# Kernel optimization log

Hardware: AMD Instinct MI355X
Metric: run time of the kernel (lower is better)

## Reference

```python
import jax, jax.numpy as jnp
import numpy as np
import math

NEG = -1000000.0

def setup_inputs() -> dict:
    key = jax.random.key(0)
    k1, k2, k3, k4 = jax.random.split(key, 4)
    B, S, D = 64, 1024, 64
    query = jax.random.normal(k1, (B, S, D), dtype=jnp.float32)
    key_t = jax.random.normal(k2, (B, S, D), dtype=jnp.float32)
    value = jax.random.normal(k3, (B, S, D), dtype=jnp.float32)
    valid_lens = jax.random.randint(k4, (B,), 1, S + 1, dtype=jnp.int32)
    return {"query": query, "key": key_t, "value": value, "valid_lens": valid_lens}

def reference(query, key, value, valid_lens):
    # query/key/value: [B, S, D]; valid_lens: [B]
    d = query.shape[-1]
    scores = jnp.einsum('bqd,bkd->bqk', query, key) / math.sqrt(d)
    Sk = key.shape[1]
    # 1D valid_lens -> same mask for every query row (repeat_interleave semantics)
    mask = jnp.arange(Sk)[None, None, :] < valid_lens[:, None, None]  # [B,1,Sk]
    scores = jnp.where(mask, scores, NEG)
    weights = jax.nn.softmax(scores, axis=-1)
    # dropout p=0.0 -> identity
    return jnp.einsum('bqk,bkd->bqd', weights, value)
```

## Files before the change

### kernel.cpp

```cpp
#include <hip/hip_runtime.h>
#include <hip/hip_bf16.h>
#include <cstdint>


typedef __attribute__((ext_vector_type(8))) short short8;
typedef __attribute__((ext_vector_type(4))) float f32x4;

#define B_   64
#define S_   1024
#define D_   64
#define BQ   64
#define BK   64
#define KPAD 72

__device__ __forceinline__ uint32_t pk2(float a, float b) {
    float2 t; t.x = a; t.y = b;
    union { __hip_bfloat162 h; uint32_t u; } c;
    c.h = __float22bfloat162_rn(t);
    return c.u;
}

__global__ __launch_bounds__(256, 4)
void attn_fwd(const float* __restrict__ Q, const float* __restrict__ K,
              const float* __restrict__ V, const int* __restrict__ VL,
              float* __restrict__ Out) {
    __shared__ __align__(16) unsigned short lK [BK * KPAD];
    __shared__ __align__(16) unsigned short lVt[D_ * 64];
    __shared__ __align__(16) unsigned short lP [4 * 16 * KPAD];
    __shared__ int sRank[64];

    const int tid  = threadIdx.x;
    const int wave = tid >> 6;
    const int lane = tid & 63;
    const int col  = lane & 15;
    const int quad = lane >> 4;

    const int g  = blockIdx.x;
    const int x  = g & 7;
    const int w  = g >> 3;
    const int pm = x * 4 + (w & 3);
    const int q0 = (w >> 2) * BQ;

    if (tid < 64) {
        const int myv = VL[tid];
        int r = 0;
        #pragma unroll 1
        for (int j = 0; j < 64; ++j) {
            const int vj = __shfl(myv, j, 64);
            r += (vj > myv) || (vj == myv && j < tid);
        }
        sRank[r] = tid;
    }
    __syncthreads();
    const int bA = sRank[pm];
    const int bB = sRank[63 - pm];

    const int T  = tid >> 4;
    const int m  = tid & 15;
    const int Tl = T & 3;
    const int cb = T >> 2;
    const int dcs = m >> 1;
    const int sws = ((dcs & 1) << 2) | (dcs >> 1);

    const float cexp = 0.18033688011112042f;
    unsigned short* pw = &lP[wave * 16 * KPAD];

    #pragma unroll 1
    for (int side = 0; side < 2; ++side) {
        const int b    = side ? bB : bA;
        const int vlen = VL[b];
        const int ntiles = (vlen + BK - 1) / BK;

        const float* Kb = K + (size_t)b * S_ * D_ + 4 * m;
        const float* Vb = V + (size_t)b * S_ * D_ + 4 * m;

        float4 kr[4], vr[4];
        #pragma unroll
        for (int j = 0; j < 4; ++j) {
            const int row = 2 * T + (j >> 1) * 32 + (j & 1);
            kr[j] = *(const float4*)(Kb + (size_t)row * D_);
            vr[j] = *(const float4*)(Vb + (size_t)row * D_);
        }

        short8 qa[2];
        {
            const int qrow = q0 + wave * 16 + col;
            const float* qp = Q + ((size_t)b * S_ + qrow) * D_ + quad * 8;
            #pragma unroll
            for (int c = 0; c < 2; ++c) {
                float4 x0 = *(const float4*)(qp + c * 32);
                float4 x1 = *(const float4*)(qp + c * 32 + 4);
                union { uint32_t u[4]; short8 s; } qq;
                qq.u[0] = pk2(x0.x, x0.y);
                qq.u[1] = pk2(x0.z, x0.w);
                qq.u[2] = pk2(x1.x, x1.y);
                qq.u[3] = pk2(x1.z, x1.w);
                qa[c] = qq.s;
            }
        }

        f32x4 ofrag[4];
        #pragma unroll
        for (int dt = 0; dt < 4; ++dt) ofrag[dt] = (f32x4){0.f, 0.f, 0.f, 0.f};
        float lsum = 0.f;

        #pragma unroll 1
        for (int kt = 0; kt < ntiles; ++kt) {
            const int kbase = kt * BK;

            __syncthreads();

            #pragma unroll
            for (int j = 0; j < 4; ++j) {
                const int row = 2 * T + (j >> 1) * 32 + (j & 1);
                uint2 kv;
                kv.x = pk2(kr[j].x, kr[j].y);
                kv.y = pk2(kr[j].z, kr[j].w);
                *(uint2*)&lK[row * KPAD + 4 * m] = kv;
            }
            #pragma unroll
            for (int i = 0; i < 2; ++i) {
                const int p = (cb + 4 * i) ^ sws;
                unsigned short* base = &lVt[p * 8 + 2 * Tl];
                const float4 va = vr[2 * i], vb2 = vr[2 * i + 1];
                *(uint32_t*)&base[(4 * m + 0) * 64] = pk2(va.x, vb2.x);
                *(uint32_t*)&base[(4 * m + 1) * 64] = pk2(va.y, vb2.y);
                *(uint32_t*)&base[(4 * m + 2) * 64] = pk2(va.z, vb2.z);
                *(uint32_t*)&base[(4 * m + 3) * 64] = pk2(va.w, vb2.w);
            }

            if (kt + 1 < ntiles) {
                const size_t off = (size_t)(kt + 1) * BK * D_;
                #pragma unroll
                for (int j = 0; j < 4; ++j) {
                    const int row = 2 * T + (j >> 1) * 32 + (j & 1);
                    kr[j] = *(const float4*)(Kb + off + (size_t)row * D_);
                    vr[j] = *(const float4*)(Vb + off + (size_t)row * D_);
                }
            }

            __syncthreads();

            f32x4 sfrag[4];
            #pragma unroll
            for (int ct = 0; ct < 4; ++ct) {
                f32x4 acc = (f32x4){0.f, 0.f, 0.f, 0.f};
                #pragma unroll
                for (int c = 0; c < 2; ++c) {
                    short8 kf = *(const short8*)&lK[(ct * 16 + col) * KPAD + c * 32 + quad * 8];
                    acc = __builtin_amdgcn_mfma_f32_16x16x32_bf16(kf, qa[c], acc, 0, 0, 0);
                }
                sfrag[ct] = acc;
            }

            if (kbase + BK <= vlen) {
                #pragma unroll
                for (int ct = 0; ct < 4; ++ct) {
                    float e0 = __builtin_amdgcn_exp2f(sfrag[ct][0] * cexp);
                    float e1 = __builtin_amdgcn_exp2f(sfrag[ct][1] * cexp);
                    float e2 = __builtin_amdgcn_exp2f(sfrag[ct][2] * cexp);
                    float e3 = __builtin_amdgcn_exp2f(sfrag[ct][3] * cexp);
                    lsum += (e0 + e1) + (e2 + e3);
                    uint2 pk; pk.x = pk2(e0, e1); pk.y = pk2(e2, e3);
                    *(uint2*)&pw[col * KPAD + ct * 16 + quad * 4] = pk;
                }
            } else {
                #pragma unroll
                for (int ct = 0; ct < 4; ++ct) {
                    const int kv0 = kbase + ct * 16 + quad * 4;
                    float e[4];
                    #pragma unroll
                    for (int rr = 0; rr < 4; ++rr) {
                        e[rr] = (kv0 + rr < vlen)
                              ? __builtin_amdgcn_exp2f(sfrag[ct][rr] * cexp) : 0.0f;
                        lsum += e[rr];
                    }
                    uint2 pk; pk.x = pk2(e[0], e[1]); pk.y = pk2(e[2], e[3]);
                    *(uint2*)&pw[col * KPAD + ct * 16 + quad * 4] = pk;
                }
            }

            #pragma unroll
            for (int kc = 0; kc < 2; ++kc) {
                short8 pa = *(const short8*)&pw[col * KPAD + kc * 32 + quad * 8];
                #pragma unroll
                for (int dt = 0; dt < 4; ++dt) {
                    const int sr = ((col >> 3) << 2) | dt;
                    const int p  = (kc * 4 + quad) ^ sr;
                    short8 vb = *(const short8*)&lVt[(dt * 16 + col) * 64 + p * 8];
                    ofrag[dt] = __builtin_amdgcn_mfma_f32_16x16x32_bf16(pa, vb, ofrag[dt], 0, 0, 0);
                }
            }
        }

        float s = lsum;
        s += __shfl_xor(s, 16, 64);
        s += __shfl_xor(s, 32, 64);
        const int qrow0 = q0 + wave * 16 + quad * 4;
        #pragma unroll
        for (int rr = 0; rr < 4; ++rr) {
            const float inv = 1.0f / __shfl(s, quad * 4 + rr, 64);
            float* op = Out + ((size_t)b * S_ + qrow0 + rr) * D_ + col;
            #pragma unroll
            for (int dt = 0; dt < 4; ++dt)
                op[dt * 16] = ofrag[dt][rr] * inv;
        }
    }
}

extern "C" void kernel_launch(void* const* d_in, const int* in_sizes, int n_in,
                              void* d_out, int out_size, void* d_ws, size_t ws_size,
                              hipStream_t stream) {
    const float* Q  = (const float*)d_in[0];
    const float* K  = (const float*)d_in[1];
    const float* V  = (const float*)d_in[2];
    const int*   VL = (const int*)d_in[3];
    float* Out = (float*)d_out;
    dim3 grid(B_ * (S_ / BQ) / 2);
    attn_fwd<<<grid, 256, 0, stream>>>(Q, K, V, VL, Out);
}
```

Baseline: 119.2 us.

## Split paired-batch blocks into one batch per block and double the grid

Each block used to process two batches (the longest and the shortest, chosen by valid_len rank) one after the other. Now each block handles a single batch, and the grid doubles to 1024 blocks. The new index mapping still interleaves batches by rank. The prefetch of the next K/V tile moves after the second barrier, and the tile loop is no longer marked unroll 1. Smaller blocks give the scheduler more freedom, but load balance now relies on hardware scheduling rather than explicit pairing.

```diff
diff --git a/kernel.cpp b/kernel.cpp
--- a/kernel.cpp
+++ b/kernel.cpp
@@ -35,12 +35,6 @@
     const int col  = lane & 15;
     const int quad = lane >> 4;
 
-    const int g  = blockIdx.x;
-    const int x  = g & 7;
-    const int w  = g >> 3;
-    const int pm = x * 4 + (w & 3);
-    const int q0 = (w >> 2) * BQ;
-
     if (tid < 64) {
         const int myv = VL[tid];
         int r = 0;
@@ -52,159 +46,159 @@
         sRank[r] = tid;
     }
     __syncthreads();
-    const int bA = sRank[pm];
-    const int bB = sRank[63 - pm];
+
+    const int g    = blockIdx.x;
+    const int x    = g & 7;
+    const int c    = (g >> 3) & 31;
+    const int s    = g >> 8;
+    const int m    = 4 * x + (c & 3);
+    const int b    = (s & 1) ? sRank[63 - m] : sRank[m];
+    const int q0   = ((c >> 2) + 8 * (s >> 1)) * BQ;
+    const int vlen = VL[b];
+    const int ntiles = (vlen + BK - 1) / BK;
 
     const int T  = tid >> 4;
-    const int m  = tid & 15;
+    const int md = tid & 15;
     const int Tl = T & 3;
     const int cb = T >> 2;
-    const int dcs = m >> 1;
+    const int dcs = md >> 1;
     const int sws = ((dcs & 1) << 2) | (dcs >> 1);
+
+    const float* Kb = K + (size_t)b * S_ * D_ + 4 * md;
+    const float* Vb = V + (size_t)b * S_ * D_ + 4 * md;
+
+    float4 kr[4], vr[4];
+    #pragma unroll
+    for (int j = 0; j < 4; ++j) {
+        const int row = 2 * T + (j >> 1) * 32 + (j & 1);
+        kr[j] = *(const float4*)(Kb + (size_t)row * D_);
+        vr[j] = *(const float4*)(Vb + (size_t)row * D_);
+    }
+
+    short8 qa[2];
+    {
+        const int qrow = q0 + wave * 16 + col;
+        const float* qp = Q + ((size_t)b * S_ + qrow) * D_ + quad * 8;
+        #pragma unroll
+        for (int cc = 0; cc < 2; ++cc) {
+            float4 x0 = *(const float4*)(qp + cc * 32);
+            float4 x1 = *(const float4*)(qp + cc * 32 + 4);
+            union { uint32_t u[4]; short8 s8; } qq;
+            qq.u[0] = pk2(x0.x, x0.y);
+            qq.u[1] = pk2(x0.z, x0.w);
+            qq.u[2] = pk2(x1.x, x1.y);
+            qq.u[3] = pk2(x1.z, x1.w);
+            qa[cc] = qq.s8;
+        }
+    }
+
+    f32x4 ofrag[4];
+    #pragma unroll
+    for (int dt = 0; dt < 4; ++dt) ofrag[dt] = (f32x4){0.f, 0.f, 0.f, 0.f};
+    float lsum = 0.f;
 
     const float cexp = 0.18033688011112042f;
     unsigned short* pw = &lP[wave * 16 * KPAD];
 
-    #pragma unroll 1
-    for (int side = 0; side < 2; ++side) {
-        const int b    = side ? bB : bA;
-        const int vlen = VL[b];
-        const int ntiles = (vlen + BK - 1) / BK;
-
-        const float* Kb = K + (size_t)b * S_ * D_ + 4 * m;
-        const float* Vb = V + (size_t)b * S_ * D_ + 4 * m;
-
-        float4 kr[4], vr[4];
+    for (int kt = 0; kt < ntiles; ++kt) {
+        const int kbase = kt * BK;
+
+        __syncthreads();
+
         #pragma unroll
         for (int j = 0; j < 4; ++j) {
             const int row = 2 * T + (j >> 1) * 32 + (j & 1);
-            kr[j] = *(const float4*)(Kb + (size_t)row * D_);
-            vr[j] = *(const float4*)(Vb + (size_t)row * D_);
-        }
-
-        short8 qa[2];
-        {
-            const int qrow = q0 + wave * 16 + col;
-            const float* qp = Q + ((size_t)b * S_ + qrow) * D_ + quad * 8;
-            #pragma unroll
-            for (int c = 0; c < 2; ++c) {
-                float4 x0 = *(const float4*)(qp + c * 32);
-                float4 x1 = *(const float4*)(qp + c * 32 + 4);
-                union { uint32_t u[4]; short8 s; } qq;
-                qq.u[0] = pk2(x0.x, x0.y);
-                qq.u[1] = pk2(x0.z, x0.w);
-                qq.u[2] = pk2(x1.x, x1.y);
-                qq.u[3] = pk2(x1.z, x1.w);
-                qa[c] = qq.s;
-            }
-        }
-
-        f32x4 ofrag[4];
-        #pragma unroll
-        for (int dt = 0; dt < 4; ++dt) ofrag[dt] = (f32x4){0.f, 0.f, 0.f, 0.f};
-        float lsum = 0.f;
-
-        #pragma unroll 1
-        for (int kt = 0; kt < ntiles; ++kt) {
-            const int kbase = kt * BK;
-
-            __syncthreads();
-
+            uint2 kv;
+            kv.x = pk2(kr[j].x, kr[j].y);
+            kv.y = pk2(kr[j].z, kr[j].w);
+            *(uint2*)&lK[row * KPAD + 4 * md] = kv;
+        }
+        #pragma unroll
+        for (int i = 0; i < 2; ++i) {
+            const int p = (cb + 4 * i) ^ sws;
+            unsigned short* base = &lVt[p * 8 + 2 * Tl];
+            const float4 va = vr[2 * i], vb2 = vr[2 * i + 1];
+            *(uint32_t*)&base[(4 * md + 0) * 64] = pk2(va.x, vb2.x);
+            *(uint32_t*)&base[(4 * md + 1) * 64] = pk2(va.y, vb2.y);
+            *(uint32_t*)&base[(4 * md + 2) * 64] = pk2(va.z, vb2.z);
+            *(uint32_t*)&base[(4 * md + 3) * 64] = pk2(va.w, vb2.w);
+        }
+
+        __syncthreads();
+
+        if (kt + 1 < ntiles) {
+            const size_t off = (size_t)(kt + 1) * BK * D_;
             #pragma unroll
             for (int j = 0; j < 4; ++j) {
                 const int row = 2 * T + (j >> 1) * 32 + (j & 1);
-                uint2 kv;
-                kv.x = pk2(kr[j].x, kr[j].y);
-                kv.y = pk2(kr[j].z, kr[j].w);
-                *(uint2*)&lK[row * KPAD + 4 * m] = kv;
-            }
-            #pragma unroll
-            for (int i = 0; i < 2; ++i) {
-                const int p = (cb + 4 * i) ^ sws;
-                unsigned short* base = &lVt[p * 8 + 2 * Tl];
-                const float4 va = vr[2 * i], vb2 = vr[2 * i + 1];
-                *(uint32_t*)&base[(4 * m + 0) * 64] = pk2(va.x, vb2.x);
-                *(uint32_t*)&base[(4 * m + 1) * 64] = pk2(va.y, vb2.y);
-                *(uint32_t*)&base[(4 * m + 2) * 64] = pk2(va.z, vb2.z);
-                *(uint32_t*)&base[(4 * m + 3) * 64] = pk2(va.w, vb2.w);
-            }
-
-            if (kt + 1 < ntiles) {
-                const size_t off = (size_t)(kt + 1) * BK * D_;
+                kr[j] = *(const float4*)(Kb + off + (size_t)row * D_);
+                vr[j] = *(const float4*)(Vb + off + (size_t)row * D_);
+            }
+        }
+
+        f32x4 sfrag[4];
+        #pragma unroll
+        for (int ct = 0; ct < 4; ++ct) {
+            f32x4 acc = (f32x4){0.f, 0.f, 0.f, 0.f};
+            #pragma unroll
+            for (int cc = 0; cc < 2; ++cc) {
+                short8 kf = *(const short8*)&lK[(ct * 16 + col) * KPAD + cc * 32 + quad * 8];
+                acc = __builtin_amdgcn_mfma_f32_16x16x32_bf16(kf, qa[cc], acc, 0, 0, 0);
+            }
+            sfrag[ct] = acc;
+        }
+
+        if (kbase + BK <= vlen) {
+            #pragma unroll
+            for (int ct = 0; ct < 4; ++ct) {
+                float e0 = __builtin_amdgcn_exp2f(sfrag[ct][0] * cexp);
+                float e1 = __builtin_amdgcn_exp2f(sfrag[ct][1] * cexp);
+                float e2 = __builtin_amdgcn_exp2f(sfrag[ct][2] * cexp);
+                float e3 = __builtin_amdgcn_exp2f(sfrag[ct][3] * cexp);
+                lsum += (e0 + e1) + (e2 + e3);
+                uint2 pk; pk.x = pk2(e0, e1); pk.y = pk2(e2, e3);
+                *(uint2*)&pw[col * KPAD + ct * 16 + quad * 4] = pk;
+            }
+        } else {
+            #pragma unroll
+            for (int ct = 0; ct < 4; ++ct) {
+                const int kv0 = kbase + ct * 16 + quad * 4;
+                float e[4];
                 #pragma unroll
-                for (int j = 0; j < 4; ++j) {
-                    const int row = 2 * T + (j >> 1) * 32 + (j & 1);
-                    kr[j] = *(const float4*)(Kb + off + (size_t)row * D_);
-                    vr[j] = *(const float4*)(Vb + off + (size_t)row * D_);
+                for (int rr = 0; rr < 4; ++rr) {
+                    e[rr] = (kv0 + rr < vlen)
+                          ? __builtin_amdgcn_exp2f(sfrag[ct][rr] * cexp) : 0.0f;
+                    lsum += e[rr];
                 }
-            }
-
-            __syncthreads();
-
-            f32x4 sfrag[4];
-            #pragma unroll
-            for (int ct = 0; ct < 4; ++ct) {
-                f32x4 acc = (f32x4){0.f, 0.f, 0.f, 0.f};
-                #pragma unroll
-                for (int c = 0; c < 2; ++c) {
-                    short8 kf = *(const short8*)&lK[(ct * 16 + col) * KPAD + c * 32 + quad * 8];
-                    acc = __builtin_amdgcn_mfma_f32_16x16x32_bf16(kf, qa[c], acc, 0, 0, 0);
-                }
-                sfrag[ct] = acc;
-            }
-
-            if (kbase + BK <= vlen) {
-                #pragma unroll
-                for (int ct = 0; ct < 4; ++ct) {
-                    float e0 = __builtin_amdgcn_exp2f(sfrag[ct][0] * cexp);
-                    float e1 = __builtin_amdgcn_exp2f(sfrag[ct][1] * cexp);
-                    float e2 = __builtin_amdgcn_exp2f(sfrag[ct][2] * cexp);
-                    float e3 = __builtin_amdgcn_exp2f(sfrag[ct][3] * cexp);
-                    lsum += (e0 + e1) + (e2 + e3);
-                    uint2 pk; pk.x = pk2(e0, e1); pk.y = pk2(e2, e3);
-                    *(uint2*)&pw[col * KPAD + ct * 16 + quad * 4] = pk;
-                }
-            } else {
-                #pragma unroll
-                for (int ct = 0; ct < 4; ++ct) {
-                    const int kv0 = kbase + ct * 16 + quad * 4;
-                    float e[4];
-                    #pragma unroll
-                    for (int rr = 0; rr < 4; ++rr) {
-                        e[rr] = (kv0 + rr < vlen)
-                              ? __builtin_amdgcn_exp2f(sfrag[ct][rr] * cexp) : 0.0f;
-                        lsum += e[rr];
-                    }
-                    uint2 pk; pk.x = pk2(e[0], e[1]); pk.y = pk2(e[2], e[3]);
-                    *(uint2*)&pw[col * KPAD + ct * 16 + quad * 4] = pk;
-                }
-            }
-
-            #pragma unroll
-            for (int kc = 0; kc < 2; ++kc) {
-                short8 pa = *(const short8*)&pw[col * KPAD + kc * 32 + quad * 8];
-                #pragma unroll
-                for (int dt = 0; dt < 4; ++dt) {
-                    const int sr = ((col >> 3) << 2) | dt;
-                    const int p  = (kc * 4 + quad) ^ sr;
-                    short8 vb = *(const short8*)&lVt[(dt * 16 + col) * 64 + p * 8];
-                    ofrag[dt] = __builtin_amdgcn_mfma_f32_16x16x32_bf16(pa, vb, ofrag[dt], 0, 0, 0);
-                }
-            }
-        }
-
-        float s = lsum;
-        s += __shfl_xor(s, 16, 64);
-        s += __shfl_xor(s, 32, 64);
-        const int qrow0 = q0 + wave * 16 + quad * 4;
-        #pragma unroll
-        for (int rr = 0; rr < 4; ++rr) {
-            const float inv = 1.0f / __shfl(s, quad * 4 + rr, 64);
-            float* op = Out + ((size_t)b * S_ + qrow0 + rr) * D_ + col;
-            #pragma unroll
-            for (int dt = 0; dt < 4; ++dt)
-                op[dt * 16] = ofrag[dt][rr] * inv;
-        }
+                uint2 pk; pk.x = pk2(e[0], e[1]); pk.y = pk2(e[2], e[3]);
+                *(uint2*)&pw[col * KPAD + ct * 16 + quad * 4] = pk;
+            }
+        }
+
+        #pragma unroll
+        for (int kc = 0; kc < 2; ++kc) {
+            short8 pa = *(const short8*)&pw[col * KPAD + kc * 32 + quad * 8];
+            #pragma unroll
+            for (int dt = 0; dt < 4; ++dt) {
+                const int sr = ((col >> 3) << 2) | dt;
+                const int p  = (kc * 4 + quad) ^ sr;
+                short8 vb = *(const short8*)&lVt[(dt * 16 + col) * 64 + p * 8];
+                ofrag[dt] = __builtin_amdgcn_mfma_f32_16x16x32_bf16(pa, vb, ofrag[dt], 0, 0, 0);
+            }
+        }
+    }
+
+    float sred = lsum;
+    sred += __shfl_xor(sred, 16, 64);
+    sred += __shfl_xor(sred, 32, 64);
+    const int qrow0 = q0 + wave * 16 + quad * 4;
+    #pragma unroll
+    for (int rr = 0; rr < 4; ++rr) {
+        const float inv = 1.0f / __shfl(sred, quad * 4 + rr, 64);
+        float* op = Out + ((size_t)b * S_ + qrow0 + rr) * D_ + col;
+        #pragma unroll
+        for (int dt = 0; dt < 4; ++dt)
+            op[dt * 16] = ofrag[dt][rr] * inv;
     }
 }
 
@@ -216,6 +210,6 @@
     const float* V  = (const float*)d_in[2];
     const int*   VL = (const int*)d_in[3];
     float* Out = (float*)d_out;
-    dim3 grid(B_ * (S_ / BQ) / 2);
+    dim3 grid(B_ * (S_ / BQ));
     attn_fwd<<<grid, 256, 0, stream>>>(Q, K, V, VL, Out);
 }
```

New measurement: 113.1 us. 1.05x faster.
